# Performance work log

Measured on AMD Instinct MI355X. Metric: run time of the kernel, lower is better.

The kernel has to match this reference:

```python
import jax, jax.numpy as jnp
import numpy as np

GRAD_WIDTH = 0.5  # PeriodicExponential defaults in sinabs
GRAD_SCALE = 1.0

B, T, C_IN, C_OUT = 100, 500, 300, 500


def setup_inputs() -> dict:
    key = jax.random.key(0)
    k1, k2, k3 = jax.random.split(key, 3)
    x = jax.random.normal(k1, (B, T, C_IN), dtype=jnp.float32)
    W = jax.random.normal(k2, (C_OUT, C_IN), dtype=jnp.float32) / np.sqrt(C_IN).astype(np.float32)
    alpha = jax.random.uniform(k3, (B * C_OUT,), dtype=jnp.float32)  # decay in [0,1)
    return {"x": x, "W": W, "alpha": alpha}


def _periodic_exp_pdf(v_mem, threshold):
    # sinabs.activation.PeriodicExponential surrogate gradient
    vs = v_mem - threshold / 2
    vper = vs - threshold * jnp.floor(vs / threshold)
    vnew = jnp.where(v_mem < threshold, vs, vper)
    return GRAD_SCALE / GRAD_WIDTH * jnp.exp(-jnp.abs(vnew - threshold / 2) / GRAD_WIDTH)


@jax.custom_vjp
def spike_fn(v_pre, threshold):
    # multi-spike: floor(v/theta) spikes when above threshold (max_num_spikes=None)
    return jnp.where(v_pre >= threshold, jnp.floor(v_pre / threshold), 0.0)


def _spike_fwd(v_pre, threshold):
    return spike_fn(v_pre, threshold), (v_pre, threshold)


def _spike_bwd(res, g):
    v_pre, threshold = res
    return (g * _periodic_exp_pdf(v_pre, threshold), jnp.zeros_like(threshold))


spike_fn.defvjp(_spike_fwd, _spike_bwd)


def _lif_forward(x, W, alpha):
    threshold = jnp.ones_like(alpha)
    v_init = jnp.zeros_like(alpha)
    # Linear (no bias): [B,T,Cin] @ [Cout,Cin]^T -> [B,T,Cout]
    x_lin = jnp.einsum('btc,oc->bto', x, W)
    # movedim(1,-1).flatten(0,1) -> neurons [B*Cout], time-major for scan: [T, B*Cout]
    inp = x_lin.transpose(1, 0, 2).reshape(T, B * C_OUT)

    def step(v, x_t):
        v_pre = alpha * v + x_t                      # leaky integrate
        v_pre = jnp.maximum(v_pre, -threshold)       # lower bound min_v_mem = -threshold
        s = spike_fn(v_pre, threshold)               # fire (multi-spike)
        v_post = v_pre - threshold * s               # reset by membrane subtraction
        return v_post, s

    _, spikes = jax.lax.scan(step, v_init, inp)      # spikes: [T, B*Cout]
    # reshape(B, Cout, T).movedim(-1, 1) -> [B, T, Cout]
    return spikes.reshape(T, B, C_OUT).transpose(1, 0, 2)


def reference(x, W, alpha):
    return _lif_forward(x, W, alpha)
```

## Files before the change

kernel.cpp:

```cpp
#include <hip/hip_runtime.h>
#include <hip/hip_bf16.h>
#include <stdint.h>

#define NB 100
#define NT 500
#define CIN 300
#define COUT 500
#define M_TOT (NB * NT)
#define MTILES 391
#define NTILES 4
#define KTILES 10
#define KT16 19
#define NPANEL (MTILES * KTILES + NTILES * KTILES)
#define WS_NEED ((size_t)NPANEL * 4096 * 4)

__device__ __forceinline__ void gload_lds16(const void* g, void* l) {
    __builtin_amdgcn_global_load_lds(
        (const __attribute__((address_space(1))) unsigned int*)g,
        (__attribute__((address_space(3))) unsigned int*)l,
        16, 0, 0);
}

__global__ __launch_bounds__(256) void split_t(
    const float* __restrict__ X, const float* __restrict__ W, float* __restrict__ ws)
{
    const int bid = blockIdx.x;
    const int tid = threadIdx.x;
    const float* src; int rowbase, nrows, kt;
    if (bid < MTILES * KTILES) {
        src = X; rowbase = (bid / KTILES) * 128; nrows = M_TOT; kt = bid % KTILES;
    } else {
        const int w = bid - MTILES * KTILES;
        src = W; rowbase = (w / KTILES) * 128; nrows = COUT; kt = w % KTILES;
    }
    const int kk = tid >> 3;
    const int m0 = (tid & 7) * 16;
    const int k  = kt * 32 + kk;

    float v[16];
    #pragma unroll
    for (int j = 0; j < 16; ++j) {
        const int row = rowbase + m0 + j;
        v[j] = (row < nrows && k < CIN) ? src[(size_t)row * CIN + k] : 0.f;
    }
    float* out = ws + (size_t)bid * 4096 + (size_t)kk * 128 + m0;
    #pragma unroll
    for (int c = 0; c < 4; ++c)
        *(float4*)(out + c * 4) = make_float4(v[c*4], v[c*4+1], v[c*4+2], v[c*4+3]);
}

__global__ __launch_bounds__(256) void gemm_t(
    const float* __restrict__ ws, float* __restrict__ C)
{
    __shared__ __align__(16) float As[3][16][128];
    __shared__ __align__(16) float Bs[3][16][128];

    const int mtile = blockIdx.x >> 2;
    const int ntile = blockIdx.x & 3;
    const int m0 = mtile * 128, n0 = ntile * 128;

    const int tid  = threadIdx.x;
    const int lane = tid & 63;
    const int wid  = tid >> 6;
    const int wmb  = (wid >> 1) << 6;
    const int wnb  = (wid & 1) << 6;
    const int r4   = (lane >> 3) << 2;
    const int c4   = (lane & 7) << 2;

    const float* Ap = ws + (size_t)(mtile * KTILES) * 4096;
    const float* Bp = ws + (size_t)(MTILES * KTILES + ntile * KTILES) * 4096;

    float acc[8][8];
    #pragma unroll
    for (int i = 0; i < 8; ++i)
        #pragma unroll
        for (int j = 0; j < 8; ++j) acc[i][j] = 0.f;

    auto stage = [&](int buf, int kt) {
        const size_t poff = (size_t)(kt >> 1) * 4096 + (size_t)(kt & 1) * 2048 + tid * 4;
        const float* xs = Ap + poff;
        const float* bs = Bp + poff;
        #pragma unroll
        for (int c = 0; c < 2; ++c) {
            gload_lds16(xs + c * 1024, (char*)&As[buf][0][0] + (size_t)(c * 256 + tid) * 16);
            gload_lds16(bs + c * 1024, (char*)&Bs[buf][0][0] + (size_t)(c * 256 + tid) * 16);
        }
    };

    stage(0, 0);
    stage(1, 1);
    asm volatile("s_waitcnt vmcnt(4)" ::: "memory");
    __builtin_amdgcn_s_barrier();
    asm volatile("" ::: "memory");

    for (int kt = 0; kt < KT16; ++kt) {
        const int cur = kt % 3;
        if (kt + 2 < KT16) stage((kt + 2) % 3, kt + 2);

        #pragma unroll 8
        for (int k = 0; k < 16; ++k) {
            float4 a0 = *(const float4*)&As[cur][k][wmb + r4];
            float4 a1 = *(const float4*)&As[cur][k][wmb + 32 + r4];
            float4 b0 = *(const float4*)&Bs[cur][k][wnb + c4];
            float4 b1 = *(const float4*)&Bs[cur][k][wnb + 32 + c4];
            float a[8] = {a0.x, a0.y, a0.z, a0.w, a1.x, a1.y, a1.z, a1.w};
            float b[8] = {b0.x, b0.y, b0.z, b0.w, b1.x, b1.y, b1.z, b1.w};
            #pragma unroll
            for (int i = 0; i < 8; ++i)
                #pragma unroll
                for (int j = 0; j < 8; ++j)
                    acc[i][j] += a[i] * b[j];
        }

        if (kt < KT16 - 1) {
            if (kt + 2 < KT16) asm volatile("s_waitcnt vmcnt(4)" ::: "memory");
            else               asm volatile("s_waitcnt vmcnt(0)" ::: "memory");
            __builtin_amdgcn_s_barrier();
            asm volatile("" ::: "memory");
        }
    }

    #pragma unroll
    for (int h = 0; h < 2; ++h) {
        #pragma unroll
        for (int i = 0; i < 4; ++i) {
            const int m = m0 + wmb + h * 32 + r4 + i;
            if (m >= M_TOT) continue;
            float* cp = C + (size_t)m * COUT;
            const int col0 = n0 + wnb + c4;
            const int col1 = col0 + 32;
            const int ai = h * 4 + i;
            if (col0 < COUT)
                *(float4*)(cp + col0) = make_float4(acc[ai][0], acc[ai][1], acc[ai][2], acc[ai][3]);
            if (col1 < COUT)
                *(float4*)(cp + col1) = make_float4(acc[ai][4], acc[ai][5], acc[ai][6], acc[ai][7]);
        }
    }
}

constexpr int BM = 128, BN = 128, BK = 32;
constexpr int LDA = BM + 4;

__global__ __launch_bounds__(256) void gemm_f32(
    const float* __restrict__ X, const float* __restrict__ W, float* __restrict__ C)
{
    __shared__ float As[BK][LDA];
    __shared__ float Bs[BK][LDA];

    const int mtile = blockIdx.x >> 2;
    const int ntile = blockIdx.x & 3;
    const int m0 = mtile * BM, n0 = ntile * BN;

    const int tid  = threadIdx.x;
    const int lane = tid & 63;
    const int wid  = tid >> 6;
    const int wmb  = (wid >> 1) << 6;
    const int wnb  = (wid & 1) << 6;
    const int r4   = (lane >> 3) << 2;
    const int c4   = (lane & 7) << 2;
    const int lr = tid >> 3;
    const int lk = (tid & 7) << 2;

    float acc[8][8];
    #pragma unroll
    for (int i = 0; i < 8; ++i)
        #pragma unroll
        for (int j = 0; j < 8; ++j) acc[i][j] = 0.f;

    for (int k0 = 0; k0 < CIN; k0 += BK) {
        const int kk = k0 + lk;
        const bool kv = (kk < CIN);
        #pragma unroll
        for (int p = 0; p < 4; ++p) {
            int row = p * 32 + lr;
            int m = m0 + row;
            float4 v = make_float4(0.f, 0.f, 0.f, 0.f);
            if (kv && m < M_TOT) v = *(const float4*)(X + (size_t)m * CIN + kk);
            As[lk + 0][row] = v.x; As[lk + 1][row] = v.y;
            As[lk + 2][row] = v.z; As[lk + 3][row] = v.w;
        }
        #pragma unroll
        for (int p = 0; p < 4; ++p) {
            int row = p * 32 + lr;
            int o = n0 + row;
            float4 v = make_float4(0.f, 0.f, 0.f, 0.f);
            if (kv && o < COUT) v = *(const float4*)(W + (size_t)o * CIN + kk);
            Bs[lk + 0][row] = v.x; Bs[lk + 1][row] = v.y;
            Bs[lk + 2][row] = v.z; Bs[lk + 3][row] = v.w;
        }
        __syncthreads();
        #pragma unroll 8
        for (int k = 0; k < BK; ++k) {
            float4 a0 = *(const float4*)&As[k][wmb + r4];
            float4 a1 = *(const float4*)&As[k][wmb + 32 + r4];
            float4 b0 = *(const float4*)&Bs[k][wnb + c4];
            float4 b1 = *(const float4*)&Bs[k][wnb + 32 + c4];
            float a[8] = {a0.x, a0.y, a0.z, a0.w, a1.x, a1.y, a1.z, a1.w};
            float b[8] = {b0.x, b0.y, b0.z, b0.w, b1.x, b1.y, b1.z, b1.w};
            #pragma unroll
            for (int i = 0; i < 8; ++i)
                #pragma unroll
                for (int j = 0; j < 8; ++j)
                    acc[i][j] += a[i] * b[j];
        }
        __syncthreads();
    }

    #pragma unroll
    for (int h = 0; h < 2; ++h) {
        #pragma unroll
        for (int i = 0; i < 4; ++i) {
            const int m = m0 + wmb + h * 32 + r4 + i;
            if (m >= M_TOT) continue;
            float* cp = C + (size_t)m * COUT;
            const int col0 = n0 + wnb + c4;
            const int col1 = col0 + 32;
            const int ai = h * 4 + i;
            if (col0 < COUT)
                *(float4*)(cp + col0) = make_float4(acc[ai][0], acc[ai][1], acc[ai][2], acc[ai][3]);
            if (col1 < COUT)
                *(float4*)(cp + col1) = make_float4(acc[ai][4], acc[ai][5], acc[ai][6], acc[ai][7]);
        }
    }
}

__global__ __launch_bounds__(256) void lif_scan(
    const float* __restrict__ alpha, float* __restrict__ C)
{
    const int n = blockIdx.x * blockDim.x + threadIdx.x;
    if (n >= NB * COUT) return;
    const int b = n / COUT, o = n % COUT;
    const float a = alpha[n];
    float v = 0.f;
    float* p = C + (size_t)b * NT * COUT + o;

    constexpr int U = 10;
    for (int t0 = 0; t0 < NT; t0 += U) {
        float xl[U];
        #pragma unroll
        for (int u = 0; u < U; ++u) xl[u] = p[(size_t)(t0 + u) * COUT];
        float s[U];
        #pragma unroll
        for (int u = 0; u < U; ++u) {
            float vp = a * v + xl[u];
            vp = fmaxf(vp, -1.f);
            float sp = (vp >= 1.f) ? floorf(vp) : 0.f;
            v = vp - sp;
            s[u] = sp;
        }
        #pragma unroll
        for (int u = 0; u < U; ++u) p[(size_t)(t0 + u) * COUT] = s[u];
    }
}

extern "C" void kernel_launch(void* const* d_in, const int* in_sizes, int n_in,
                              void* d_out, int out_size, void* d_ws, size_t ws_size,
                              hipStream_t stream) {
    const float* X     = (const float*)d_in[0];
    const float* W     = (const float*)d_in[1];
    const float* alpha = (const float*)d_in[2];
    float* C = (float*)d_out;

    if (ws_size >= WS_NEED && d_ws != nullptr) {
        float* ws = (float*)d_ws;
        split_t<<<dim3(NPANEL), dim3(256), 0, stream>>>(X, W, ws);
        gemm_t<<<dim3(MTILES * NTILES), dim3(256), 0, stream>>>(ws, C);
    } else {
        gemm_f32<<<dim3(MTILES * 4), dim3(256), 0, stream>>>(X, W, C);
    }

    const int nneur = NB * COUT;
    lif_scan<<<dim3((nneur + 255) / 256), dim3(256), 0, stream>>>(alpha, C);
}
```

Measured before the change: 289.4 us.

## Give each wave private LDS double buffers to drop block-wide barriers in GEMM

The shared triple-buffered A/B LDS tiles are replaced with per-wave double buffers. Each wave async-loads only the 64-wide A and B slices it needs, so the loop synchronises with per-wave vmcnt waits instead of workgroup s_barrier calls. This removes barrier stalls between waves. In exchange, each A/B slice is loaded twice from global memory because two waves share it, LDS use rises to 64KB per block, and pipelining drops from three stages to two.

```diff
diff --git a/kernel.cpp b/kernel.cpp
--- a/kernel.cpp
+++ b/kernel.cpp
@@ -52,8 +52,8 @@
 __global__ __launch_bounds__(256) void gemm_t(
     const float* __restrict__ ws, float* __restrict__ C)
 {
-    __shared__ __align__(16) float As[3][16][128];
-    __shared__ __align__(16) float Bs[3][16][128];
+    __shared__ __align__(16) float Aw[4][2][16][64];
+    __shared__ __align__(16) float Bw[4][2][16][64];
 
     const int mtile = blockIdx.x >> 2;
     const int ntile = blockIdx.x & 3;
@@ -70,6 +70,11 @@
     const float* Ap = ws + (size_t)(mtile * KTILES) * 4096;
     const float* Bp = ws + (size_t)(MTILES * KTILES + ntile * KTILES) * 4096;
 
+    const int kl = lane >> 4;
+    const int mq = lane & 15;
+    const int aoff = kl * 128 + wmb + mq * 4;
+    const int boff = kl * 128 + wnb + mq * 4;
+
     float acc[8][8];
     #pragma unroll
     for (int i = 0; i < 8; ++i)
@@ -77,32 +82,32 @@
         for (int j = 0; j < 8; ++j) acc[i][j] = 0.f;
 
     auto stage = [&](int buf, int kt) {
-        const size_t poff = (size_t)(kt >> 1) * 4096 + (size_t)(kt & 1) * 2048 + tid * 4;
-        const float* xs = Ap + poff;
-        const float* bs = Bp + poff;
-        #pragma unroll
-        for (int c = 0; c < 2; ++c) {
-            gload_lds16(xs + c * 1024, (char*)&As[buf][0][0] + (size_t)(c * 256 + tid) * 16);
-            gload_lds16(bs + c * 1024, (char*)&Bs[buf][0][0] + (size_t)(c * 256 + tid) * 16);
+        const size_t tileoff = (size_t)(kt >> 1) * 4096 + (size_t)(kt & 1) * 2048;
+        const float* xa = Ap + tileoff + aoff;
+        const float* xb = Bp + tileoff + boff;
+        char* la = (char*)&Aw[wid][buf][0][0] + lane * 16;
+        char* lb = (char*)&Bw[wid][buf][0][0] + lane * 16;
+        #pragma unroll
+        for (int c = 0; c < 4; ++c) {
+            gload_lds16(xa + c * 512, la + c * 1024);
+            gload_lds16(xb + c * 512, lb + c * 1024);
         }
     };
 
     stage(0, 0);
     stage(1, 1);
-    asm volatile("s_waitcnt vmcnt(4)" ::: "memory");
-    __builtin_amdgcn_s_barrier();
-    asm volatile("" ::: "memory");
 
     for (int kt = 0; kt < KT16; ++kt) {
-        const int cur = kt % 3;
-        if (kt + 2 < KT16) stage((kt + 2) % 3, kt + 2);
+        const int cur = kt & 1;
+        if (kt < KT16 - 1) asm volatile("s_waitcnt vmcnt(8)" ::: "memory");
+        else               asm volatile("s_waitcnt vmcnt(0)" ::: "memory");
 
         #pragma unroll 8
         for (int k = 0; k < 16; ++k) {
-            float4 a0 = *(const float4*)&As[cur][k][wmb + r4];
-            float4 a1 = *(const float4*)&As[cur][k][wmb + 32 + r4];
-            float4 b0 = *(const float4*)&Bs[cur][k][wnb + c4];
-            float4 b1 = *(const float4*)&Bs[cur][k][wnb + 32 + c4];
+            float4 a0 = *(const float4*)&Aw[wid][cur][k][r4];
+            float4 a1 = *(const float4*)&Aw[wid][cur][k][32 + r4];
+            float4 b0 = *(const float4*)&Bw[wid][cur][k][c4];
+            float4 b1 = *(const float4*)&Bw[wid][cur][k][32 + c4];
             float a[8] = {a0.x, a0.y, a0.z, a0.w, a1.x, a1.y, a1.z, a1.w};
             float b[8] = {b0.x, b0.y, b0.z, b0.w, b1.x, b1.y, b1.z, b1.w};
             #pragma unroll
@@ -112,12 +117,7 @@
                     acc[i][j] += a[i] * b[j];
         }
 
-        if (kt < KT16 - 1) {
-            if (kt + 2 < KT16) asm volatile("s_waitcnt vmcnt(4)" ::: "memory");
-            else               asm volatile("s_waitcnt vmcnt(0)" ::: "memory");
-            __builtin_amdgcn_s_barrier();
-            asm volatile("" ::: "memory");
-        }
+        if (kt + 2 < KT16) stage(cur, kt + 2);
     }
 
     #pragma unroll
```

Measured after the change: 284.8 us. Within noise of the previous version (-1.6%).
